# Kernel optimization log

Hardware: AMD Instinct MI355X
Metric: run time of the kernel (lower is better)

Reference implementation:

```python
import jax, jax.numpy as jnp
import numpy as np

B_SZ = 64            # oft_block_size
IN_F = 4096
OUT_F = 4096
R_IN = IN_F // B_SZ   # 64 blocks
R_OUT = OUT_F // B_SZ # 64 blocks
N_TRI = B_SZ * (B_SZ - 1) // 2  # 2016 packed strict-upper entries
NUM_NEUMANN = 5

_rows, _cols = np.triu_indices(B_SZ, k=1)
ROWS = jnp.asarray(_rows, dtype=jnp.int32)
COLS = jnp.asarray(_cols, dtype=jnp.int32)


def setup_inputs() -> dict:
    key = jax.random.key(0)
    k = jax.random.split(key, 5)
    x = jax.random.normal(k[0], (4, 2048, IN_F), dtype=jnp.float32)
    # small skew entries so the Neumann series approximates the Cayley transform
    Ro = jax.random.normal(k[1], (R_OUT, N_TRI), dtype=jnp.float32) * 0.01
    Ri = jax.random.normal(k[2], (R_IN, N_TRI), dtype=jnp.float32) * 0.01
    W = jax.random.normal(k[3], (OUT_F, IN_F), dtype=jnp.float32) * (1.0 / np.sqrt(IN_F))
    bias = jax.random.normal(k[4], (OUT_F,), dtype=jnp.float32) * 0.01
    rng = np.random.default_rng(0)
    perm_in = rng.permutation(IN_F)
    perm_in_inv = np.argsort(perm_in)
    perm_out = rng.permutation(OUT_F)
    return {
        "x": x, "Ro": Ro, "Ri": Ri, "W": W, "bias": bias,
        "perm_in_inv": jnp.asarray(perm_in_inv, dtype=jnp.int32),
        "perm_out": jnp.asarray(perm_out, dtype=jnp.int32),
    }


def _skew(vec):
    # vec: (r, n_tri) packed strict-upper entries -> (r, b, b) skew-symmetric
    r = vec.shape[0]
    M = jnp.zeros((r, B_SZ, B_SZ), dtype=vec.dtype).at[:, ROWS, COLS].set(vec)
    return M - jnp.swapaxes(M, -2, -1)


def _cayley_neumann(Q):
    # R = I + 2*(Q + Q^2 + Q^3 + Q^4)   (num_neumann_terms = 5)
    I = jnp.eye(B_SZ, dtype=Q.dtype)
    acc = Q
    Qp = Q
    for _ in range(3, NUM_NEUMANN):
        pass
    Q2 = jnp.matmul(Q, Q)
    acc = acc + Q2
    Qp = Q2
    for _ in range(3, NUM_NEUMANN):
        Qp = jnp.matmul(Qp, Q)
        acc = acc + Qp
    return I + 2.0 * acc


def reference(x, Ro, Ri, W, bias, perm_in_inv, perm_out):
    R_out = _cayley_neumann(_skew(Ro))   # (r_out, b, b)
    R_in = _cayley_neumann(_skew(Ri))    # (r_in, b, b)

    B, S, _ = x.shape
    xp = x[..., perm_in_inv]                               # input permutation
    xb = xp.reshape(B, S, R_IN, B_SZ)
    xR = jnp.einsum('bsrc,rcd->bsrd', xb, R_in)            # block-diag right rotate
    y = xR.reshape(B, S, IN_F) @ W.T + bias                # base linear
    yb = y.reshape(B, S, R_OUT, B_SZ)
    yR = jnp.einsum('bsrc,rcd->bsrd', yb, R_out)           # block-diag output rotate
    out = yR.reshape(B, S, OUT_F)[..., perm_out]           # output permutation
    return out
```

## Files before the change

kernel.cpp:

```cpp
#include <hip/hip_runtime.h>
#include <stdint.h>

#define IN_F 4096
#define OUT_F 4096
#define NTRI 2016

typedef unsigned short u16;
typedef __attribute__((ext_vector_type(8))) short short8;
typedef __attribute__((ext_vector_type(4))) float f32x4;
typedef __attribute__((ext_vector_type(4))) int i32x4;
typedef __attribute__((ext_vector_type(4))) unsigned short u16x4;

__device__ __forceinline__ u16 f2bf(float f) {
    uint32_t u = __builtin_bit_cast(uint32_t, f);
    u = (u + 0x7FFFu + ((u >> 16) & 1u)) >> 16;
    return (u16)u;
}

__device__ __forceinline__ void gload16(const void* g, void* l) {
    __builtin_amdgcn_global_load_lds((__attribute__((address_space(1))) void*)g,
                                     (__attribute__((address_space(3))) void*)l,
                                     16, 0, 0);
}

__global__ __launch_bounds__(256) void k_prep(const float* __restrict__ Ro,
                                              const float* __restrict__ Ri,
                                              const int* __restrict__ perm_out,
                                              const float* __restrict__ x,
                                              const int* __restrict__ pii,
                                              float* __restrict__ Rout,
                                              u16* __restrict__ QT16,
                                              u16* __restrict__ P16,
                                              int* __restrict__ pinv_out,
                                              u16* __restrict__ xb) {
    const int b = blockIdx.x;
    const int t = threadIdx.x;
    if (b == 128) {
#pragma unroll
        for (int e = 0; e < 16; ++e) {
            int i = e * 256 + t;
            pinv_out[perm_out[i]] = i;
        }
        return;
    }
    if (b >= 129) {
        __shared__ __align__(16) float xr[4096];
        const int blk = b - 129;
        int pv[16];
#pragma unroll
        for (int q = 0; q < 4; ++q) *(i32x4*)&pv[q * 4] = *(const i32x4*)&pii[t * 16 + q * 4];
        for (int r = 0; r < 8; ++r) {
            size_t srow = (size_t)blk * 8 + r;
            const float* src = x + srow * 4096;
#pragma unroll
            for (int q = 0; q < 4; ++q)
                *(f32x4*)&xr[q * 1024 + t * 4] = *(const f32x4*)&src[q * 1024 + t * 4];
            __syncthreads();
            union { short8 v; u16 e[8]; } o0, o1;
#pragma unroll
            for (int j = 0; j < 8; ++j) { o0.e[j] = f2bf(xr[pv[j]]); o1.e[j] = f2bf(xr[pv[8 + j]]); }
            *(short8*)&xb[srow * 4096 + t * 16] = o0.v;
            *(short8*)&xb[srow * 4096 + t * 16 + 8] = o1.v;
            __syncthreads();
        }
        return;
    }
    __shared__ __align__(16) float Qs[64 * 64];
    __shared__ __align__(16) float Ps[64 * 68];
    __shared__ __align__(16) float Ts[64 * 68];
    const float* vec = (b < 64) ? (Ro + (size_t)b * NTRI) : (Ri + (size_t)(b - 64) * NTRI);
    int tr = t >> 4, tc = t & 15;
#pragma unroll
    for (int e = 0; e < 16; ++e) {
        int el = e * 256 + t;
        int i = el >> 6, j = el & 63;
        float q = 0.f;
        if (i < j) q =  vec[i * 63 - (i * (i - 1)) / 2 + (j - i - 1)];
        if (i > j) q = -vec[j * 63 - (j * (j - 1)) / 2 + (i - j - 1)];
        Qs[el] = q;
    }
    __syncthreads();
    float a2[4][4], a3[4][4], a4[4][4];
#pragma unroll
    for (int i = 0; i < 4; ++i)
#pragma unroll
        for (int j = 0; j < 4; ++j) { a2[i][j] = 0.f; a3[i][j] = 0.f; a4[i][j] = 0.f; }
    for (int k = 0; k < 64; ++k) {
        f32x4 qa = *(const f32x4*)&Qs[k * 64 + tr * 4];
        f32x4 qb = *(const f32x4*)&Qs[k * 64 + tc * 4];
#pragma unroll
        for (int i = 0; i < 4; ++i)
#pragma unroll
            for (int j = 0; j < 4; ++j) a2[i][j] -= qa[i] * qb[j];
    }
#pragma unroll
    for (int i = 0; i < 4; ++i)
#pragma unroll
        for (int j = 0; j < 4; ++j) Ps[(tr * 4 + i) * 68 + tc * 4 + j] = a2[i][j];
    __syncthreads();
    for (int k = 0; k < 64; ++k) {
        f32x4 pa = *(const f32x4*)&Ps[k * 68 + tr * 4];
        f32x4 qb = *(const f32x4*)&Qs[k * 64 + tc * 4];
#pragma unroll
        for (int i = 0; i < 4; ++i)
#pragma unroll
            for (int j = 0; j < 4; ++j) a3[i][j] += pa[i] * qb[j];
    }
#pragma unroll
    for (int i = 0; i < 4; ++i)
#pragma unroll
        for (int j = 0; j < 4; ++j) Ts[(tc * 4 + j) * 68 + tr * 4 + i] = -a3[i][j];
    __syncthreads();
    for (int k = 0; k < 64; ++k) {
        f32x4 ta = *(const f32x4*)&Ts[k * 68 + tr * 4];
        f32x4 qb = *(const f32x4*)&Qs[k * 64 + tc * 4];
#pragma unroll
        for (int i = 0; i < 4; ++i)
#pragma unroll
            for (int j = 0; j < 4; ++j) a4[i][j] -= ta[i] * qb[j];
    }
    if (b < 64) {
        float* dst = Rout + (size_t)b * 4096;
        u16* qt = QT16 + (size_t)b * 4096;
#pragma unroll
        for (int i = 0; i < 4; ++i) {
            int gi = tr * 4 + i;
            f32x4 q4 = *(const f32x4*)&Qs[gi * 64 + tc * 4];
            f32x4 o;
#pragma unroll
            for (int j = 0; j < 4; ++j) {
                int gj = tc * 4 + j;
                o[j] = 2.f * (q4[j] + a2[i][j] + a3[i][j] + a4[i][j]) + ((gi == gj) ? 1.f : 0.f);
            }
            *(f32x4*)&dst[gi * 64 + tc * 4] = o;
#pragma unroll
            for (int j = 0; j < 4; ++j) qt[(tc * 4 + j) * 64 + gi] = f2bf(o[j]);
        }
    } else {
        u16* p = P16 + (size_t)(b - 64) * 4096;
#pragma unroll
        for (int i = 0; i < 4; ++i) {
            int gi = tr * 4 + i;
            f32x4 q4 = *(const f32x4*)&Qs[gi * 64 + tc * 4];
            u16x4 pk;
#pragma unroll
            for (int j = 0; j < 4; ++j) {
                int gj = tc * 4 + j;
                float v = 2.f * (q4[j] + a2[i][j] + a3[i][j] + a4[i][j]) + ((gi == gj) ? 1.f : 0.f);
                pk[j] = f2bf(v);
            }
            *(u16x4*)&p[gi * 64 + tc * 4] = pk;
        }
    }
}

__global__ __launch_bounds__(256) void k_work(const float* __restrict__ W,
                                              const u16* __restrict__ P16,
                                              const u16* __restrict__ QT16,
                                              const int* __restrict__ pinv_out,
                                              const float* __restrict__ bias,
                                              const float* __restrict__ Rout,
                                              const int* __restrict__ perm_out,
                                              u16* __restrict__ Ctp,
                                              float* __restrict__ bfinal) {
    const int fb = blockIdx.x;
    const int t = threadIdx.x;
    if (fb < 2048) {
        __shared__ __align__(16) u16 Wst[128 * 64];
        __shared__ __align__(16) u16 Ut[64 * 128];
        const int s = fb & 63;
        const int br = fb >> 6;
        const int lane = t & 63;
        const int w = t >> 6;
        const int fl = lane & 15;
        const int kg = lane >> 4;

        short8 bfP[4][2];
        const u16* Pbase = P16 + (size_t)s * 4096;
#pragma unroll
        for (int nf = 0; nf < 4; ++nf)
#pragma unroll
            for (int kk = 0; kk < 2; ++kk)
                bfP[nf][kk] = *(const short8*)(Pbase + (nf * 16 + fl) * 64 + kk * 32 + kg * 8);

#pragma unroll
        for (int q = 0; q < 4; ++q) {
            int ci = q * 256 + t;
            int row = ci >> 3, slot = ci & 7;
            const float* src = W + (size_t)(br * 128 + row) * IN_F + s * 64 + slot * 8;
            f32x4 v0 = *(const f32x4*)src;
            f32x4 v1 = *(const f32x4*)(src + 4);
            union { short8 v; u16 e[8]; } cv;
            cv.e[0] = f2bf(v0[0]); cv.e[1] = f2bf(v0[1]); cv.e[2] = f2bf(v0[2]); cv.e[3] = f2bf(v0[3]);
            cv.e[4] = f2bf(v1[0]); cv.e[5] = f2bf(v1[1]); cv.e[6] = f2bf(v1[2]); cv.e[7] = f2bf(v1[3]);
            *(short8*)&Wst[row * 64 + (slot ^ (row & 7)) * 8] = cv.v;
        }
        __syncthreads();

        f32x4 acc1[2][4];
#pragma unroll
        for (int mf = 0; mf < 2; ++mf)
#pragma unroll
            for (int nf = 0; nf < 4; ++nf) acc1[mf][nf] = f32x4{0.f, 0.f, 0.f, 0.f};
#pragma unroll
        for (int mf = 0; mf < 2; ++mf) {
            int row = w * 32 + mf * 16 + fl;
#pragma unroll
            for (int kk = 0; kk < 2; ++kk) {
                short8 a = *(const short8*)&Wst[row * 64 + ((kk * 4 + kg) ^ (row & 7)) * 8];
#pragma unroll
                for (int nf = 0; nf < 4; ++nf)
                    acc1[mf][nf] = __builtin_amdgcn_mfma_f32_16x16x32_bf16(a, bfP[nf][kk], acc1[mf][nf], 0, 0, 0);
            }
        }
#pragma unroll
        for (int mf = 0; mf < 2; ++mf)
#pragma unroll
            for (int nf = 0; nf < 4; ++nf) {
                int i = nf * 16 + fl;
                int c = w * 32 + mf * 16 + kg * 4;
                u16x4 pk;
#pragma unroll
                for (int reg = 0; reg < 4; ++reg) pk[reg] = f2bf(acc1[mf][nf][reg]);
                int slot = c >> 3, half = (c >> 2) & 1;
                *(u16x4*)&Ut[i * 128 + ((slot ^ (i & 7)) << 3) + (half << 2)] = pk;
            }
        __syncthreads();

        const int rbl = w >> 1;
        const int r_g = br * 2 + rbl;
        short8 aQ[2][2];
#pragma unroll
        for (int mf2 = 0; mf2 < 2; ++mf2) {
            int d = (w & 1) * 32 + mf2 * 16 + fl;
#pragma unroll
            for (int kk = 0; kk < 2; ++kk)
                aQ[mf2][kk] = *(const short8*)(QT16 + (size_t)r_g * 4096 + d * 64 + kk * 32 + kg * 8);
        }
        f32x4 acc2[2][4];
#pragma unroll
        for (int mf2 = 0; mf2 < 2; ++mf2)
#pragma unroll
            for (int nf = 0; nf < 4; ++nf) acc2[mf2][nf] = f32x4{0.f, 0.f, 0.f, 0.f};
#pragma unroll
        for (int kk = 0; kk < 2; ++kk)
#pragma unroll
            for (int nf = 0; nf < 4; ++nf) {
                int i = nf * 16 + fl;
                int slot = rbl * 8 + kk * 4 + kg;
                short8 bu = *(const short8*)&Ut[i * 128 + ((slot ^ (i & 7)) << 3)];
#pragma unroll
                for (int mf2 = 0; mf2 < 2; ++mf2)
                    acc2[mf2][nf] = __builtin_amdgcn_mfma_f32_16x16x32_bf16(aQ[mf2][kk], bu, acc2[mf2][nf], 0, 0, 0);
            }
#pragma unroll
        for (int mf2 = 0; mf2 < 2; ++mf2)
#pragma unroll
            for (int reg = 0; reg < 4; ++reg) {
                int o_g = br * 128 + w * 32 + mf2 * 16 + kg * 4 + reg;
                int j = pinv_out[o_g];
                u16* dst = Ctp + (size_t)j * IN_F + s * 64;
#pragma unroll
                for (int nf = 0; nf < 4; ++nf)
                    dst[nf * 16 + fl] = f2bf(acc2[mf2][nf][reg]);
            }
    } else {
        int j = (fb - 2048) * 256 + t;
        int o = perm_out[j];
        int r = o >> 6, d = o & 63;
        const float* Rb = Rout + (size_t)r * 4096;
        const float* bb = bias + r * 64;
        float s = 0.f;
        for (int c = 0; c < 64; ++c) s += bb[c] * Rb[c * 64 + d];
        bfinal[j] = s;
    }
}

__global__ __launch_bounds__(512, 2) void k_gemm(const u16* __restrict__ A,
                                                 const u16* __restrict__ Bt,
                                                 const float* __restrict__ bias,
                                                 float* __restrict__ out) {
    __shared__ __align__(16) u16 lds[65536];
    const int t = threadIdx.x;
    const int lane = t & 63;
    const int wid = t >> 6;
    const int wr = wid >> 2, wc = wid & 3;

    int flat = blockIdx.y * gridDim.x + blockIdx.x;
    int swz  = (flat & 7) * 64 + (flat >> 3);
    int bm = swz >> 4;
    int bn = swz & 15;

    const int srow = t >> 2;
    const int sks  = (t & 3) ^ ((t >> 3) & 3);
    const u16* sA0 = A  + (size_t)(bm * 256 + srow) * IN_F + sks * 8;
    const u16* sA1 = sA0 + (size_t)128 * IN_F;
    const u16* sB0 = Bt + (size_t)(bn * 256 + srow) * IN_F + sks * 8;
    const u16* sB1 = sB0 + (size_t)128 * IN_F;
    u16* dA = lds + t * 8;
    u16* dB = lds + 8192 + t * 8;

    const int frow = lane & 15;
    const int kg = lane >> 4;
    const int swzr = kg ^ ((frow >> 1) & 3);
    const int aoff = (wr * 128 + frow) * 32 + swzr * 8;
    const int boff = 8192 + (wc * 64 + frow) * 32 + swzr * 8;

#define STAGE(slot, kt) do { int bb_ = (slot) * 16384, off_ = (kt) * 32; \
        gload16(sA0 + off_, dA + bb_); gload16(sA1 + off_, dA + bb_ + 4096); \
        gload16(sB0 + off_, dB + bb_); gload16(sB1 + off_, dB + bb_ + 4096); } while (0)

#define LOADFRAGS(AF, BF, buf) do { const u16* base_ = lds + (buf) * 16384; \
        _Pragma("unroll") for (int m_ = 0; m_ < 8; ++m_) AF[m_] = *(const short8*)(base_ + aoff + m_ * 512); \
        _Pragma("unroll") for (int n_ = 0; n_ < 4; ++n_) BF[n_] = *(const short8*)(base_ + boff + n_ * 512); } while (0)

#define MFMAS(AF, BF) do { __builtin_amdgcn_s_setprio(1); \
        _Pragma("unroll") for (int m_ = 0; m_ < 8; ++m_) \
        _Pragma("unroll") for (int n_ = 0; n_ < 4; ++n_) \
            acc[m_][n_] = __builtin_amdgcn_mfma_f32_16x16x32_bf16(AF[m_], BF[n_], acc[m_][n_], 0, 0, 0); \
        __builtin_amdgcn_s_setprio(0); } while (0)

    f32x4 acc[8][4];
#pragma unroll
    for (int m = 0; m < 8; ++m)
#pragma unroll
        for (int n = 0; n < 4; ++n) acc[m][n] = f32x4{0.f, 0.f, 0.f, 0.f};

    STAGE(0, 0); STAGE(1, 1); STAGE(2, 2);
    asm volatile("s_waitcnt vmcnt(4)" ::: "memory");
    __builtin_amdgcn_s_barrier();

    short8 afX[8], bfX[4], afY[8], bfY[4];
    LOADFRAGS(afX, bfX, 0);

    for (int ii = 0; ii < 64; ++ii) {
        {
            const int i = 2 * ii;
            LOADFRAGS(afY, bfY, (i + 1) & 3);
            int ts = i + 3; if (ts > 127) ts = 127;
            STAGE((i + 3) & 3, ts);
            MFMAS(afX, bfX);
            asm volatile("s_waitcnt vmcnt(4)" ::: "memory");
            __builtin_amdgcn_s_barrier();
        }
        {
            const int i = 2 * ii + 1;
            LOADFRAGS(afX, bfX, (i + 1) & 3);
            int ts = i + 3; if (ts > 127) ts = 127;
            STAGE((i + 3) & 3, ts);
            MFMAS(afY, bfY);
            asm volatile("s_waitcnt vmcnt(4)" ::: "memory");
            __builtin_amdgcn_s_barrier();
        }
    }
    asm volatile("s_waitcnt vmcnt(0)" ::: "memory");

    const int col0 = bn * 256 + wc * 64 + frow;
    const int row0 = bm * 256 + wr * 128 + kg * 4;
    float bv[4];
#pragma unroll
    for (int n = 0; n < 4; ++n) bv[n] = bias[col0 + n * 16];
#pragma unroll
    for (int m = 0; m < 8; ++m)
#pragma unroll
        for (int n = 0; n < 4; ++n)
#pragma unroll
            for (int i = 0; i < 4; ++i)
                out[(size_t)(row0 + m * 16 + i) * OUT_F + col0 + n * 16] = acc[m][n][i] + bv[n];
#undef STAGE
#undef LOADFRAGS
#undef MFMAS
}

extern "C" void kernel_launch(void* const* d_in, const int* in_sizes, int n_in,
                              void* d_out, int out_size, void* d_ws, size_t ws_size,
                              hipStream_t stream) {
    (void)in_sizes; (void)n_in; (void)out_size; (void)ws_size;
    const float* x    = (const float*)d_in[0];
    const float* Ro   = (const float*)d_in[1];
    const float* Ri   = (const float*)d_in[2];
    const float* W    = (const float*)d_in[3];
    const float* bias = (const float*)d_in[4];
    const int* perm_in_inv = (const int*)d_in[5];
    const int* perm_out    = (const int*)d_in[6];
    float* out = (float*)d_out;

    char* ws = (char*)d_ws;
    float* Rout   = (float*)(ws);
    u16*   P16    = (u16*)(ws + (1ull << 20));
    u16*   QT16   = (u16*)(ws + (1ull << 20) + (1 << 19));
    int*   pinvo  = (int*)(ws + (2ull << 20));
    float* bfinal = (float*)(ws + (2ull << 20) + (1 << 16));
    u16*   Ctp    = (u16*)(ws + (4ull << 20));
    u16*   xb     = (u16*)(ws + (36ull << 20));

    k_prep<<<1153, 256, 0, stream>>>(Ro, Ri, perm_out, x, perm_in_inv,
                                     Rout, QT16, P16, pinvo, xb);
    k_work<<<2064, 256, 0, stream>>>(W, P16, QT16, pinvo, bias, Rout,
                                     perm_out, Ctp, bfinal);
    k_gemm<<<dim3(16, 32), 512, 0, stream>>>(xb, Ctp, bfinal, out);
}
```

Before: 313.2 us.

## Load B fragments directly from global memory instead of staging through LDS

Only the A tile is staged through LDS now. Each wave loads its B MFMA fragments straight from global memory into registers one k-step ahead, and LDS use drops by half. The aim is to cut LDS traffic and footprint for the B operand. The trade-off is that B rows are no longer shared across the two wave rows, so global/L2 reads of B double. The vmcnt accounting also becomes harder to get right, since register loads of B now share the counter with the A DMA loads.

```diff
diff --git a/kernel.cpp b/kernel.cpp
--- a/kernel.cpp
+++ b/kernel.cpp
@@ -280,7 +280,7 @@
                                                  const u16* __restrict__ Bt,
                                                  const float* __restrict__ bias,
                                                  float* __restrict__ out) {
-    __shared__ __align__(16) u16 lds[65536];
+    __shared__ __align__(16) u16 lds[32768];
     const int t = threadIdx.x;
     const int lane = t & 63;
     const int wid = t >> 6;
@@ -295,24 +295,23 @@
     const int sks  = (t & 3) ^ ((t >> 3) & 3);
     const u16* sA0 = A  + (size_t)(bm * 256 + srow) * IN_F + sks * 8;
     const u16* sA1 = sA0 + (size_t)128 * IN_F;
-    const u16* sB0 = Bt + (size_t)(bn * 256 + srow) * IN_F + sks * 8;
-    const u16* sB1 = sB0 + (size_t)128 * IN_F;
     u16* dA = lds + t * 8;
-    u16* dB = lds + 8192 + t * 8;
 
     const int frow = lane & 15;
     const int kg = lane >> 4;
     const int swzr = kg ^ ((frow >> 1) & 3);
     const int aoff = (wr * 128 + frow) * 32 + swzr * 8;
-    const int boff = 8192 + (wc * 64 + frow) * 32 + swzr * 8;
-
-#define STAGE(slot, kt) do { int bb_ = (slot) * 16384, off_ = (kt) * 32; \
-        gload16(sA0 + off_, dA + bb_); gload16(sA1 + off_, dA + bb_ + 4096); \
-        gload16(sB0 + off_, dB + bb_); gload16(sB1 + off_, dB + bb_ + 4096); } while (0)
-
-#define LOADFRAGS(AF, BF, buf) do { const u16* base_ = lds + (buf) * 16384; \
-        _Pragma("unroll") for (int m_ = 0; m_ < 8; ++m_) AF[m_] = *(const short8*)(base_ + aoff + m_ * 512); \
-        _Pragma("unroll") for (int n_ = 0; n_ < 4; ++n_) BF[n_] = *(const short8*)(base_ + boff + n_ * 512); } while (0)
+
+    const u16* gBf = Bt + (size_t)(bn * 256 + wc * 64 + frow) * IN_F + kg * 8;
+
+#define STAGE(slot, kt) do { u16* d_ = dA + (slot) * 8192; int off_ = (kt) * 32; \
+        gload16(sA0 + off_, d_); gload16(sA1 + off_, d_ + 4096); } while (0)
+
+#define LOADA(AF, buf) do { const u16* base_ = lds + (buf) * 8192 + aoff; \
+        _Pragma("unroll") for (int m_ = 0; m_ < 8; ++m_) AF[m_] = *(const short8*)(base_ + m_ * 512); } while (0)
+
+#define LOADB(BF, kt) do { const u16* b_ = gBf + (size_t)(kt) * 32; \
+        _Pragma("unroll") for (int n_ = 0; n_ < 4; ++n_) BF[n_] = *(const short8*)(b_ + (size_t)(n_ * 16) * IN_F); } while (0)
 
 #define MFMAS(AF, BF) do { __builtin_amdgcn_s_setprio(1); \
         _Pragma("unroll") for (int m_ = 0; m_ < 8; ++m_) \
@@ -327,29 +326,34 @@
         for (int n = 0; n < 4; ++n) acc[m][n] = f32x4{0.f, 0.f, 0.f, 0.f};
 
     STAGE(0, 0); STAGE(1, 1); STAGE(2, 2);
-    asm volatile("s_waitcnt vmcnt(4)" ::: "memory");
+    asm volatile("s_waitcnt vmcnt(2)" ::: "memory");
     __builtin_amdgcn_s_barrier();
 
-    short8 afX[8], bfX[4], afY[8], bfY[4];
-    LOADFRAGS(afX, bfX, 0);
+    short8 afX[8], afY[8], bfX[4], bfY[4];
+    LOADA(afX, 0);
+    LOADB(bfX, 0);
 
     for (int ii = 0; ii < 64; ++ii) {
         {
             const int i = 2 * ii;
-            LOADFRAGS(afY, bfY, (i + 1) & 3);
+            int kn = i + 1; if (kn > 127) kn = 127;
+            LOADB(bfY, kn);
+            LOADA(afY, (i + 1) & 3);
             int ts = i + 3; if (ts > 127) ts = 127;
             STAGE((i + 3) & 3, ts);
             MFMAS(afX, bfX);
-            asm volatile("s_waitcnt vmcnt(4)" ::: "memory");
+            asm volatile("s_waitcnt vmcnt(6)" ::: "memory");
             __builtin_amdgcn_s_barrier();
         }
         {
             const int i = 2 * ii + 1;
-            LOADFRAGS(afX, bfX, (i + 1) & 3);
+            int kn = i + 1; if (kn > 127) kn = 127;
+            LOADB(bfX, kn);
+            LOADA(afX, (i + 1) & 3);
             int ts = i + 3; if (ts > 127) ts = 127;
             STAGE((i + 3) & 3, ts);
             MFMAS(afY, bfY);
-            asm volatile("s_waitcnt vmcnt(4)" ::: "memory");
+            asm volatile("s_waitcnt vmcnt(6)" ::: "memory");
             __builtin_amdgcn_s_barrier();
         }
     }
@@ -368,7 +372,8 @@
             for (int i = 0; i < 4; ++i)
                 out[(size_t)(row0 + m * 16 + i) * OUT_F + col0 + n * 16] = acc[m][n][i] + bv[n];
 #undef STAGE
-#undef LOADFRAGS
+#undef LOADA
+#undef LOADB
 #undef MFMAS
 }
 
```

Result: slower. 453.0 us (+44.6%).

## Switch GEMM to 32x32x16 bf16 MFMA with matching LDS swizzle

Applied to the files above, without the earlier changes.

Replaces the 16x16x32 MFMA tiling in the main GEMM with 32x32x16 bf16 MFMAs, reorganizing the per-wave fragment layout (4x2 tiles of 32x32 instead of 8x4 of 16x16). The LDS staging swizzle and fragment read offsets are redone to suit the new operand layout, and the epilogue is rewritten for the 32x32 accumulator layout. The aim is higher MFMA throughput per instruction and fewer LDS fragment reads per K step. Risks are LDS bank conflicts under the new swizzle and epilogue store coalescing.

```diff
diff --git a/kernel.cpp b/kernel.cpp
--- a/kernel.cpp
+++ b/kernel.cpp
@@ -8,6 +8,7 @@
 typedef unsigned short u16;
 typedef __attribute__((ext_vector_type(8))) short short8;
 typedef __attribute__((ext_vector_type(4))) float f32x4;
+typedef __attribute__((ext_vector_type(16))) float f32x16;
 typedef __attribute__((ext_vector_type(4))) int i32x4;
 typedef __attribute__((ext_vector_type(4))) unsigned short u16x4;
 
@@ -291,46 +292,54 @@
     int bm = swz >> 4;
     int bn = swz & 15;
 
-    const int srow = t >> 2;
-    const int sks  = (t & 3) ^ ((t >> 3) & 3);
-    const u16* sA0 = A  + (size_t)(bm * 256 + srow) * IN_F + sks * 8;
+    const int ska = ((t & 3) + 4 - ((t >> 5) & 3)) & 3;
+    const u16* sA0 = A  + (size_t)(bm * 256 + (t >> 2)) * IN_F + ska * 8;
     const u16* sA1 = sA0 + (size_t)128 * IN_F;
-    const u16* sB0 = Bt + (size_t)(bn * 256 + srow) * IN_F + sks * 8;
+    const u16* sB0 = Bt + (size_t)(bn * 256 + (t >> 2)) * IN_F + ska * 8;
     const u16* sB1 = sB0 + (size_t)128 * IN_F;
     u16* dA = lds + t * 8;
     u16* dB = lds + 8192 + t * 8;
 
-    const int frow = lane & 15;
-    const int kg = lane >> 4;
-    const int swzr = kg ^ ((frow >> 1) & 3);
-    const int aoff = (wr * 128 + frow) * 32 + swzr * 8;
-    const int boff = 8192 + (wc * 64 + frow) * 32 + swzr * 8;
+    const int cl = lane & 31;
+    const int kh = lane >> 5;
+    int fs[2];
+    fs[0] = ((0 + kh + (cl >> 3)) & 3) * 8;
+    fs[1] = ((2 + kh + (cl >> 3)) & 3) * 8;
+    const int abase = wr * 4096 + cl * 32;
+    const int bbase = 8192 + (wc >> 1) * 4096 + (wc & 1) * 2048 + cl * 32;
 
 #define STAGE(slot, kt) do { int bb_ = (slot) * 16384, off_ = (kt) * 32; \
         gload16(sA0 + off_, dA + bb_); gload16(sA1 + off_, dA + bb_ + 4096); \
         gload16(sB0 + off_, dB + bb_); gload16(sB1 + off_, dB + bb_ + 4096); } while (0)
 
 #define LOADFRAGS(AF, BF, buf) do { const u16* base_ = lds + (buf) * 16384; \
-        _Pragma("unroll") for (int m_ = 0; m_ < 8; ++m_) AF[m_] = *(const short8*)(base_ + aoff + m_ * 512); \
-        _Pragma("unroll") for (int n_ = 0; n_ < 4; ++n_) BF[n_] = *(const short8*)(base_ + boff + n_ * 512); } while (0)
+        _Pragma("unroll") for (int m_ = 0; m_ < 4; ++m_) \
+        _Pragma("unroll") for (int k_ = 0; k_ < 2; ++k_) \
+            AF[m_][k_] = *(const short8*)(base_ + abase + m_ * 1024 + fs[k_]); \
+        _Pragma("unroll") for (int n_ = 0; n_ < 2; ++n_) \
+        _Pragma("unroll") for (int k_ = 0; k_ < 2; ++k_) \
+            BF[n_][k_] = *(const short8*)(base_ + bbase + n_ * 1024 + fs[k_]); } while (0)
 
 #define MFMAS(AF, BF) do { __builtin_amdgcn_s_setprio(1); \
-        _Pragma("unroll") for (int m_ = 0; m_ < 8; ++m_) \
-        _Pragma("unroll") for (int n_ = 0; n_ < 4; ++n_) \
-            acc[m_][n_] = __builtin_amdgcn_mfma_f32_16x16x32_bf16(AF[m_], BF[n_], acc[m_][n_], 0, 0, 0); \
+        _Pragma("unroll") for (int k_ = 0; k_ < 2; ++k_) \
+        _Pragma("unroll") for (int m_ = 0; m_ < 4; ++m_) \
+        _Pragma("unroll") for (int n_ = 0; n_ < 2; ++n_) \
+            acc[m_][n_] = __builtin_amdgcn_mfma_f32_32x32x16_bf16(AF[m_][k_], BF[n_][k_], acc[m_][n_], 0, 0, 0); \
         __builtin_amdgcn_s_setprio(0); } while (0)
 
-    f32x4 acc[8][4];
-#pragma unroll
-    for (int m = 0; m < 8; ++m)
-#pragma unroll
-        for (int n = 0; n < 4; ++n) acc[m][n] = f32x4{0.f, 0.f, 0.f, 0.f};
+    f32x16 acc[4][2];
+#pragma unroll
+    for (int m = 0; m < 4; ++m)
+#pragma unroll
+        for (int n = 0; n < 2; ++n)
+#pragma unroll
+            for (int e = 0; e < 16; ++e) acc[m][n][e] = 0.f;
 
     STAGE(0, 0); STAGE(1, 1); STAGE(2, 2);
     asm volatile("s_waitcnt vmcnt(4)" ::: "memory");
     __builtin_amdgcn_s_barrier();
 
-    short8 afX[8], bfX[4], afY[8], bfY[4];
+    short8 afX[4][2], bfX[2][2], afY[4][2], bfY[2][2];
     LOADFRAGS(afX, bfX, 0);
 
     for (int ii = 0; ii < 64; ++ii) {
@@ -355,18 +364,21 @@
     }
     asm volatile("s_waitcnt vmcnt(0)" ::: "memory");
 
-    const int col0 = bn * 256 + wc * 64 + frow;
-    const int row0 = bm * 256 + wr * 128 + kg * 4;
-    float bv[4];
-#pragma unroll
-    for (int n = 0; n < 4; ++n) bv[n] = bias[col0 + n * 16];
-#pragma unroll
-    for (int m = 0; m < 8; ++m)
-#pragma unroll
-        for (int n = 0; n < 4; ++n)
-#pragma unroll
-            for (int i = 0; i < 4; ++i)
-                out[(size_t)(row0 + m * 16 + i) * OUT_F + col0 + n * 16] = acc[m][n][i] + bv[n];
+    const int row0 = bm * 256 + wr * 128 + kh * 4;
+    float bv[2];
+    bv[0] = bias[bn * 256 + wc * 64 + cl];
+    bv[1] = bias[bn * 256 + wc * 64 + 32 + cl];
+#pragma unroll
+    for (int mi = 0; mi < 4; ++mi)
+#pragma unroll
+        for (int ni = 0; ni < 2; ++ni) {
+            int col = bn * 256 + wc * 64 + ni * 32 + cl;
+#pragma unroll
+            for (int r = 0; r < 16; ++r) {
+                int row = row0 + mi * 32 + (r & 3) + 8 * (r >> 2);
+                out[(size_t)row * OUT_F + col] = acc[mi][ni][r] + bv[ni];
+            }
+        }
 #undef STAGE
 #undef LOADFRAGS
 #undef MFMAS
```

Measured after the change: 345.7 us. +10.4%, slower.
